# Performance work log

Measured on AMD Instinct MI355X. Metric: run time of the kernel, lower is better.

## Reference

```python
import jax, jax.numpy as jnp
import numpy as np

B, N, D = 2, 2048, 1024
H, DH = 16, 64
INNER = H * DH  # 1024
EPS = 1e-5


def setup_inputs() -> dict:
    key = jax.random.key(0)
    ks = jax.random.split(key, 7)
    x = jax.random.normal(ks[0], (B, N, D), dtype=jnp.float32)
    mask = jax.random.uniform(ks[1], (B, N)) < 0.9
    mask = mask.at[:, 0].set(True)  # guarantee at least one valid key per row
    attn_bias = jax.random.normal(ks[2], (H, N, N), dtype=jnp.float32) * 0.02
    ln_w = jnp.ones((D,), dtype=jnp.float32)
    ln_b = jnp.zeros((D,), dtype=jnp.float32)
    wq = jax.random.normal(ks[3], (D, INNER), dtype=jnp.float32) * 0.02
    wkv = jax.random.normal(ks[4], (D, 2 * DH), dtype=jnp.float32) * 0.02
    wo = jax.random.normal(ks[5], (INNER, D), dtype=jnp.float32) * 0.02
    return {"x": x, "attn_bias": attn_bias, "ln_w": ln_w, "ln_b": ln_b,
            "wq": wq, "wkv": wkv, "wo": wo, "mask": mask}


def reference(x, attn_bias, ln_w, ln_b, wq, wkv, wo, mask):
    scale = DH ** -0.5
    # NOTE: in the torch module, kv_input = x BEFORE self.norm (context=None),
    # so K/V come from raw x while Q comes from LayerNorm(x).
    mu = jnp.mean(x, axis=-1, keepdims=True)
    var = jnp.var(x, axis=-1, keepdims=True)
    xn = (x - mu) / jnp.sqrt(var + EPS) * ln_w + ln_b
    q = (xn @ wq).reshape(B, N, H, DH).transpose(0, 2, 1, 3) * scale  # b h n d
    kv = x @ wkv                     # b n 2*dh (shared single KV head, MQA)
    k, v = kv[..., :DH], kv[..., DH:]
    sim = jnp.einsum('bhid,bjd->bhij', q, k) + attn_bias  # bias broadcasts over b
    mask_value = -jnp.finfo(sim.dtype).max
    sim = jnp.where(mask[:, None, None, :], sim, mask_value)
    attn = jax.nn.softmax(sim, axis=-1)
    out = jnp.einsum('bhij,bjd->bhid', attn, v)
    out = out.transpose(0, 2, 1, 3).reshape(B, N, INNER)
    return out @ wo
```

## Files before the change

### kernel.cpp

```cpp
#include <hip/hip_runtime.h>
#include <hip/hip_bf16.h>

typedef __bf16 bf16_t;
typedef __bf16 bf16x4 __attribute__((ext_vector_type(4)));
typedef __bf16 bf16x8 __attribute__((ext_vector_type(8)));
typedef float f32x4 __attribute__((ext_vector_type(4)));

static constexpr int BB    = 2;
static constexpr int SEQ   = 2048;
static constexpr int DM    = 1024;
static constexpr int NHEAD = 16;
static constexpr int HD    = 64;
static constexpr float L2E = 1.4426950408889634f;

__device__ __forceinline__ bf16x8 ld8(const bf16_t* p) {
  return *reinterpret_cast<const bf16x8*>(p);
}

__device__ __forceinline__ void gl_lds16(const bf16_t* g, bf16_t* l) {
  __builtin_amdgcn_global_load_lds(
      (const __attribute__((address_space(1))) void*)g,
      (__attribute__((address_space(3))) void*)l, 16, 0, 0);
}

template <typename T> __device__ __forceinline__ T cvt_out(float v);
template <> __device__ __forceinline__ float  cvt_out<float >(float v) { return v; }
template <> __device__ __forceinline__ bf16_t cvt_out<bf16_t>(float v) { return (bf16_t)v; }

__global__ __launch_bounds__(256) void transpose_cast(const float* __restrict__ in,
                                                      bf16_t* __restrict__ out,
                                                      int R, int C) {
  __shared__ float tile[32][33];
  const int c0 = blockIdx.x * 32, r0 = blockIdx.y * 32;
  const int tx = threadIdx.x & 31, ty = threadIdx.x >> 5;
#pragma unroll
  for (int y = ty; y < 32; y += 8)
    tile[y][tx] = in[(size_t)(r0 + y) * C + (c0 + tx)];
  __syncthreads();
#pragma unroll
  for (int y = ty; y < 32; y += 8)
    out[(size_t)(c0 + y) * R + (r0 + tx)] = (bf16_t)tile[tx][y];
}

__global__ __launch_bounds__(256) void row_prep(const float* __restrict__ x,
    const float* __restrict__ ln_w, const float* __restrict__ ln_b,
    const int* __restrict__ mask,
    bf16_t* __restrict__ xbf, bf16_t* __restrict__ xn, float* __restrict__ maskA) {
  const int row = blockIdx.x, t = threadIdx.x;
  __shared__ float red[8];
  const float4 xv = *reinterpret_cast<const float4*>(&x[(size_t)row * DM + t * 4]);
  float s  = xv.x + xv.y + xv.z + xv.w;
  float s2 = xv.x * xv.x + xv.y * xv.y + xv.z * xv.z + xv.w * xv.w;
#pragma unroll
  for (int off = 32; off >= 1; off >>= 1) {
    s  += __shfl_xor(s,  off, 64);
    s2 += __shfl_xor(s2, off, 64);
  }
  if ((t & 63) == 0) { red[t >> 6] = s; red[4 + (t >> 6)] = s2; }
  __syncthreads();
  s  = red[0] + red[1] + red[2] + red[3];
  s2 = red[4] + red[5] + red[6] + red[7];
  const float mu   = s * (1.0f / DM);
  const float var  = s2 * (1.0f / DM) - mu * mu;
  const float rstd = rsqrtf(var + 1e-5f);
  const float4 wv = *reinterpret_cast<const float4*>(&ln_w[t * 4]);
  const float4 bv = *reinterpret_cast<const float4*>(&ln_b[t * 4]);
  union { bf16_t h[4]; uint2 u; } p0, p1;
  p0.h[0] = (bf16_t)xv.x; p0.h[1] = (bf16_t)xv.y;
  p0.h[2] = (bf16_t)xv.z; p0.h[3] = (bf16_t)xv.w;
  p1.h[0] = (bf16_t)((xv.x - mu) * rstd * wv.x + bv.x);
  p1.h[1] = (bf16_t)((xv.y - mu) * rstd * wv.y + bv.y);
  p1.h[2] = (bf16_t)((xv.z - mu) * rstd * wv.z + bv.z);
  p1.h[3] = (bf16_t)((xv.w - mu) * rstd * wv.w + bv.w);
  *reinterpret_cast<uint2*>(&xbf[(size_t)row * DM + t * 4]) = p0.u;
  *reinterpret_cast<uint2*>(&xn [(size_t)row * DM + t * 4]) = p1.u;
  if (t == 0) maskA[row] = mask[row] ? 0.0f : -1e30f;
}

template <typename OutT>
__global__ __launch_bounds__(256) void gemm_lds(const bf16_t* __restrict__ A,
    const bf16_t* __restrict__ Bt, OutT* __restrict__ C, OutT* __restrict__ C2,
    int M, int Nn, int K, float scale) {
  __shared__ alignas(16) bf16_t As[128 * 32];
  __shared__ alignas(16) bf16_t Bs[64 * 32];
  const int m0 = blockIdx.x * 128, n0 = blockIdx.y * 64;
  const int t = threadIdx.x, lane = t & 63, w = t >> 6;
  const int wm = (w & 1) * 64, wn = (w >> 1) * 32;
  const int l15 = lane & 15, q4 = lane >> 4;
  f32x4 acc[4][2] = {};
  const int sr = lane >> 2, sc = (lane & 3) * 8;
  const bf16_t* Ap0 = A  + (size_t)(m0 + w * 32 + sr) * K + sc;
  const bf16_t* Ap1 = Ap0 + (size_t)16 * K;
  const bf16_t* Bp  = Bt + (size_t)(n0 + w * 16 + sr) * K + sc;
  bf16_t* AsL0 = &As[(w * 32) * 32];
  bf16_t* AsL1 = &As[(w * 32 + 16) * 32];
  bf16_t* BsL  = &Bs[(w * 16) * 32];
  for (int k0 = 0; k0 < K; k0 += 32) {
    gl_lds16(Ap0 + k0, AsL0);
    gl_lds16(Ap1 + k0, AsL1);
    gl_lds16(Bp  + k0, BsL);
    __syncthreads();
    bf16x8 af[4], bfr[2];
#pragma unroll
    for (int mt = 0; mt < 4; ++mt) af[mt]  = ld8(&As[(wm + mt * 16 + l15) * 32 + q4 * 8]);
#pragma unroll
    for (int nt = 0; nt < 2; ++nt) bfr[nt] = ld8(&Bs[(wn + nt * 16 + l15) * 32 + q4 * 8]);
#pragma unroll
    for (int mt = 0; mt < 4; ++mt)
#pragma unroll
      for (int nt = 0; nt < 2; ++nt)
        acc[mt][nt] = __builtin_amdgcn_mfma_f32_16x16x32_bf16(af[mt], bfr[nt], acc[mt][nt], 0, 0, 0);
    __syncthreads();
  }
#pragma unroll
  for (int mt = 0; mt < 4; ++mt)
#pragma unroll
    for (int nt = 0; nt < 2; ++nt)
#pragma unroll
      for (int r = 0; r < 4; ++r) {
        const int gm = m0 + wm + mt * 16 + q4 * 4 + r;
        const int gn = n0 + wn + nt * 16 + l15;
        const OutT ov = cvt_out<OutT>(acc[mt][nt][r] * scale);
        if (C2 == nullptr) {
          C[(size_t)gm * Nn + gn] = ov;
        } else if (gn < HD) {
          C[(size_t)gm * HD + gn] = ov;
        } else {
          C2[((size_t)(gm >> 11) * HD + (gn - HD)) * SEQ + (gm & 2047)] = ov;
        }
      }
}

__global__ __launch_bounds__(256) void flash_attn(
    const bf16_t* __restrict__ q,
    const bf16_t* __restrict__ kk,
    const bf16_t* __restrict__ vT,
    const float*  __restrict__ bias,
    const float*  __restrict__ maskA,
    bf16_t* __restrict__ aout)
{
  const int b = blockIdx.y & 1, h = blockIdx.y >> 1;
  const int i0 = blockIdx.x * 64;
  const int t = threadIdx.x, lane = t & 63, w = t >> 6;
  const int l15 = lane & 15, q4 = lane >> 4;

  __shared__ alignas(16) bf16_t Qs[64][72];
  __shared__ alignas(16) bf16_t Ks[64][72];
  __shared__ alignas(16) bf16_t Vs[64][72];
  __shared__ alignas(16) bf16_t Pt[4][16][72];

  const int sr = t >> 2, sc = (t & 3) * 16;
  {
    const bf16_t* src = &q[((size_t)b * SEQ + i0 + sr) * DM + h * HD + sc];
    *reinterpret_cast<uint4*>(&Qs[sr][sc])     = *reinterpret_cast<const uint4*>(src);
    *reinterpret_cast<uint4*>(&Qs[sr][sc + 8]) = *reinterpret_cast<const uint4*>(src + 8);
  }
  __syncthreads();
  const bf16x8 bq0 = ld8(&Qs[w * 16 + l15][q4 * 8]);
  const bf16x8 bq1 = ld8(&Qs[w * 16 + l15][32 + q4 * 8]);

  f32x4 o[4] = {};
  float m_run = -1e30f, l_run = 0.0f;

  const float* bias_p = bias + (size_t)h * SEQ * SEQ
                      + (size_t)(i0 + w * 16 + l15) * SEQ + q4 * 4;
  const float* mask_p = maskA + b * SEQ + q4 * 4;
  const bf16_t* kp = &kk[((size_t)b * SEQ + sr) * HD + sc];
  const bf16_t* vp = &vT[((size_t)b * HD + sr) * SEQ + sc];

  for (int j0 = 0; j0 < SEQ; j0 += 64) {
    {
      const bf16_t* ks = kp + (size_t)j0 * HD;
      *reinterpret_cast<uint4*>(&Ks[sr][sc])     = *reinterpret_cast<const uint4*>(ks);
      *reinterpret_cast<uint4*>(&Ks[sr][sc + 8]) = *reinterpret_cast<const uint4*>(ks + 8);
      const bf16_t* vs = vp + j0;
      *reinterpret_cast<uint4*>(&Vs[sr][sc])     = *reinterpret_cast<const uint4*>(vs);
      *reinterpret_cast<uint4*>(&Vs[sr][sc + 8]) = *reinterpret_cast<const uint4*>(vs + 8);
    }
    f32x4 bv[4], mv[4];
#pragma unroll
    for (int mt = 0; mt < 4; ++mt) {
      bv[mt] = *reinterpret_cast<const f32x4*>(bias_p + j0 + mt * 16);
      mv[mt] = *reinterpret_cast<const f32x4*>(mask_p + j0 + mt * 16);
    }
    __syncthreads();

    f32x4 s[4];
#pragma unroll
    for (int mt = 0; mt < 4; ++mt) {
      const bf16x8 a0 = ld8(&Ks[mt * 16 + l15][q4 * 8]);
      const bf16x8 a1 = ld8(&Ks[mt * 16 + l15][32 + q4 * 8]);
      f32x4 z = {0.f, 0.f, 0.f, 0.f};
      z = __builtin_amdgcn_mfma_f32_16x16x32_bf16(a0, bq0, z, 0, 0, 0);
      z = __builtin_amdgcn_mfma_f32_16x16x32_bf16(a1, bq1, z, 0, 0, 0);
      s[mt] = z;
    }

    float mx = -1e30f;
#pragma unroll
    for (int mt = 0; mt < 4; ++mt)
#pragma unroll
      for (int r = 0; r < 4; ++r) {
        s[mt][r] = s[mt][r] + bv[mt][r] + mv[mt][r];
        mx = fmaxf(mx, s[mt][r]);
      }
    mx = fmaxf(mx, __shfl_xor(mx, 16, 64));
    mx = fmaxf(mx, __shfl_xor(mx, 32, 64));
    const float mnew  = fmaxf(m_run, mx);
    const float alpha = __builtin_amdgcn_exp2f((m_run - mnew) * L2E);
    const float cc    = -mnew * L2E;
    m_run = mnew;

    float su = 0.0f;
#pragma unroll
    for (int mt = 0; mt < 4; ++mt)
#pragma unroll
      for (int r = 0; r < 4; ++r) {
        s[mt][r] = __builtin_amdgcn_exp2f(__builtin_fmaf(s[mt][r], L2E, cc));
        su += s[mt][r];
      }
    su += __shfl_xor(su, 16, 64);
    su += __shfl_xor(su, 32, 64);
    l_run = l_run * alpha + su;

#pragma unroll
    for (int mt = 0; mt < 4; ++mt) {
      bf16x4 pk = {(bf16_t)s[mt][0], (bf16_t)s[mt][1], (bf16_t)s[mt][2], (bf16_t)s[mt][3]};
      *reinterpret_cast<bf16x4*>(&Pt[w][l15][mt * 16 + q4 * 4]) = pk;
    }

#pragma unroll
    for (int r = 0; r < 4; ++r) {
      const float a_r = __shfl(alpha, (q4 << 2) + r, 64);
      o[0][r] *= a_r; o[1][r] *= a_r; o[2][r] *= a_r; o[3][r] *= a_r;
    }

#pragma unroll
    for (int ks = 0; ks < 2; ++ks) {
      const bf16x8 pf = ld8(&Pt[w][l15][ks * 32 + q4 * 8]);
#pragma unroll
      for (int nt = 0; nt < 4; ++nt) {
        const bf16x8 vv = ld8(&Vs[nt * 16 + l15][ks * 32 + q4 * 8]);
        o[nt] = __builtin_amdgcn_mfma_f32_16x16x32_bf16(pf, vv, o[nt], 0, 0, 0);
      }
    }
    __syncthreads();
  }

#pragma unroll
  for (int r = 0; r < 4; ++r) {
    const float linv = 1.0f / __shfl(l_run, (q4 << 2) + r, 64);
    const int gi = i0 + w * 16 + q4 * 4 + r;
    bf16_t* dst = &aout[((size_t)b * SEQ + gi) * DM + h * HD];
#pragma unroll
    for (int nt = 0; nt < 4; ++nt)
      dst[nt * 16 + l15] = (bf16_t)(o[nt][r] * linv);
  }
}

extern "C" void kernel_launch(void* const* d_in, const int* in_sizes, int n_in,
                              void* d_out, int out_size, void* d_ws, size_t ws_size,
                              hipStream_t stream) {
  const float* x         = (const float*)d_in[0];
  const float* attn_bias = (const float*)d_in[1];
  const float* ln_w      = (const float*)d_in[2];
  const float* ln_b      = (const float*)d_in[3];
  const float* wq        = (const float*)d_in[4];
  const float* wkv       = (const float*)d_in[5];
  const float* wo        = (const float*)d_in[6];
  const int*   mask      = (const int*)d_in[7];
  float* out = (float*)d_out;

  char* ws = (char*)d_ws;
  size_t off = 0;
  auto alloc = [&](size_t bytes) {
    char* p = ws + off;
    off += (bytes + 255) & ~(size_t)255;
    return p;
  };
  bf16_t* xbf   = (bf16_t*)alloc((size_t)BB * SEQ * DM * 2);
  bf16_t* xn    = (bf16_t*)alloc((size_t)BB * SEQ * DM * 2);
  bf16_t* wqT   = (bf16_t*)alloc((size_t)DM * DM * 2);
  bf16_t* wkvT  = (bf16_t*)alloc((size_t)2 * HD * DM * 2);
  bf16_t* woT   = (bf16_t*)alloc((size_t)DM * DM * 2);
  bf16_t* qb    = (bf16_t*)alloc((size_t)BB * SEQ * DM * 2);
  bf16_t* kkb   = (bf16_t*)alloc((size_t)BB * SEQ * HD * 2);
  bf16_t* vTb   = (bf16_t*)alloc((size_t)BB * HD * SEQ * 2);
  bf16_t* aoutb = (bf16_t*)alloc((size_t)BB * SEQ * DM * 2);
  float*  maskA = (float*)alloc((size_t)BB * SEQ * 4);

  transpose_cast<<<dim3(DM / 32, DM / 32), 256, 0, stream>>>(wq, wqT, DM, DM);
  transpose_cast<<<dim3(128 / 32, DM / 32), 256, 0, stream>>>(wkv, wkvT, DM, 128);
  transpose_cast<<<dim3(DM / 32, DM / 32), 256, 0, stream>>>(wo, woT, DM, DM);
  row_prep<<<BB * SEQ, 256, 0, stream>>>(x, ln_w, ln_b, mask, xbf, xn, maskA);
  gemm_lds<bf16_t><<<dim3(32, 16), 256, 0, stream>>>(xn, wqT, qb, (bf16_t*)nullptr,
                                                     BB * SEQ, DM, DM, 0.125f);
  gemm_lds<bf16_t><<<dim3(32, 2), 256, 0, stream>>>(xbf, wkvT, kkb, vTb,
                                                    BB * SEQ, 128, DM, 1.0f);
  flash_attn<<<dim3(SEQ / 64, BB * NHEAD), 256, 0, stream>>>(qb, kkb, vTb, attn_bias,
                                                             maskA, aoutb);
  gemm_lds<float><<<dim3(32, 16), 256, 0, stream>>>(aoutb, woT, out, (float*)nullptr,
                                                    BB * SEQ, DM, DM, 1.0f);
}
```

Baseline: 525.9 us.

## Double-buffer K/V in flash attention, shuffle P in registers, widen GEMM tiles

New measurement: 512.2 us. -2.6%, faster.

```diff
diff --git a/kernel.cpp b/kernel.cpp
--- a/kernel.cpp
+++ b/kernel.cpp
@@ -21,6 +21,13 @@
   __builtin_amdgcn_global_load_lds(
       (const __attribute__((address_space(1))) void*)g,
       (__attribute__((address_space(3))) void*)l, 16, 0, 0);
+}
+
+__device__ __forceinline__ uint2 shfl2(uint2 v, int src) {
+  uint2 r;
+  r.x = (unsigned)__shfl((int)v.x, src, 64);
+  r.y = (unsigned)__shfl((int)v.y, src, 64);
+  return r;
 }
 
 template <typename T> __device__ __forceinline__ T cvt_out(float v);
@@ -78,9 +85,58 @@
 }
 
 template <typename OutT>
-__global__ __launch_bounds__(256) void gemm_lds(const bf16_t* __restrict__ A,
-    const bf16_t* __restrict__ Bt, OutT* __restrict__ C, OutT* __restrict__ C2,
+__global__ __launch_bounds__(256) void gemm128(const bf16_t* __restrict__ A,
+    const bf16_t* __restrict__ Bt, OutT* __restrict__ C,
     int M, int Nn, int K, float scale) {
+  __shared__ alignas(16) bf16_t As[128 * 32];
+  __shared__ alignas(16) bf16_t Bs[128 * 32];
+  const int m0 = blockIdx.x * 128, n0 = blockIdx.y * 128;
+  const int t = threadIdx.x, lane = t & 63, w = t >> 6;
+  const int wm = (w & 1) * 64, wn = (w >> 1) * 64;
+  const int l15 = lane & 15, q4 = lane >> 4;
+  f32x4 acc[4][4] = {};
+  const int sr = lane >> 2, sc = (lane & 3) * 8;
+  const bf16_t* Ap0 = A  + (size_t)(m0 + w * 32 + sr) * K + sc;
+  const bf16_t* Ap1 = Ap0 + (size_t)16 * K;
+  const bf16_t* Bp0 = Bt + (size_t)(n0 + w * 32 + sr) * K + sc;
+  const bf16_t* Bp1 = Bp0 + (size_t)16 * K;
+  bf16_t* AsL0 = &As[(w * 32) * 32];
+  bf16_t* AsL1 = &As[(w * 32 + 16) * 32];
+  bf16_t* BsL0 = &Bs[(w * 32) * 32];
+  bf16_t* BsL1 = &Bs[(w * 32 + 16) * 32];
+  for (int k0 = 0; k0 < K; k0 += 32) {
+    gl_lds16(Ap0 + k0, AsL0);
+    gl_lds16(Ap1 + k0, AsL1);
+    gl_lds16(Bp0 + k0, BsL0);
+    gl_lds16(Bp1 + k0, BsL1);
+    __syncthreads();
+    bf16x8 af[4], bfr[4];
+#pragma unroll
+    for (int mt = 0; mt < 4; ++mt) af[mt]  = ld8(&As[(wm + mt * 16 + l15) * 32 + q4 * 8]);
+#pragma unroll
+    for (int nt = 0; nt < 4; ++nt) bfr[nt] = ld8(&Bs[(wn + nt * 16 + l15) * 32 + q4 * 8]);
+#pragma unroll
+    for (int mt = 0; mt < 4; ++mt)
+#pragma unroll
+      for (int nt = 0; nt < 4; ++nt)
+        acc[mt][nt] = __builtin_amdgcn_mfma_f32_16x16x32_bf16(af[mt], bfr[nt], acc[mt][nt], 0, 0, 0);
+    __syncthreads();
+  }
+#pragma unroll
+  for (int mt = 0; mt < 4; ++mt)
+#pragma unroll
+    for (int nt = 0; nt < 4; ++nt)
+#pragma unroll
+      for (int r = 0; r < 4; ++r) {
+        const int gm = m0 + wm + mt * 16 + q4 * 4 + r;
+        const int gn = n0 + wn + nt * 16 + l15;
+        C[(size_t)gm * Nn + gn] = cvt_out<OutT>(acc[mt][nt][r] * scale);
+      }
+}
+
+__global__ __launch_bounds__(256) void gemm_kv(const bf16_t* __restrict__ A,
+    const bf16_t* __restrict__ Bt, bf16_t* __restrict__ C, bf16_t* __restrict__ C2,
+    int M, int Nn, int K) {
   __shared__ alignas(16) bf16_t As[128 * 32];
   __shared__ alignas(16) bf16_t Bs[64 * 32];
   const int m0 = blockIdx.x * 128, n0 = blockIdx.y * 64;
@@ -120,18 +176,13 @@
       for (int r = 0; r < 4; ++r) {
         const int gm = m0 + wm + mt * 16 + q4 * 4 + r;
         const int gn = n0 + wn + nt * 16 + l15;
-        const OutT ov = cvt_out<OutT>(acc[mt][nt][r] * scale);
-        if (C2 == nullptr) {
-          C[(size_t)gm * Nn + gn] = ov;
-        } else if (gn < HD) {
-          C[(size_t)gm * HD + gn] = ov;
-        } else {
-          C2[((size_t)(gm >> 11) * HD + (gn - HD)) * SEQ + (gm & 2047)] = ov;
-        }
-      }
-}
-
-__global__ __launch_bounds__(256) void flash_attn(
+        const bf16_t ov = (bf16_t)acc[mt][nt][r];
+        if (gn < HD) C[(size_t)gm * HD + gn] = ov;
+        else C2[((size_t)(gm >> 11) * HD + (gn - HD)) * SEQ + (gm & 2047)] = ov;
+      }
+}
+
+__global__ __launch_bounds__(256, 4) void flash_attn(
     const bf16_t* __restrict__ q,
     const bf16_t* __restrict__ kk,
     const bf16_t* __restrict__ vT,
@@ -144,20 +195,12 @@
   const int t = threadIdx.x, lane = t & 63, w = t >> 6;
   const int l15 = lane & 15, q4 = lane >> 4;
 
-  __shared__ alignas(16) bf16_t Qs[64][72];
-  __shared__ alignas(16) bf16_t Ks[64][72];
-  __shared__ alignas(16) bf16_t Vs[64][72];
-  __shared__ alignas(16) bf16_t Pt[4][16][72];
-
-  const int sr = t >> 2, sc = (t & 3) * 16;
-  {
-    const bf16_t* src = &q[((size_t)b * SEQ + i0 + sr) * DM + h * HD + sc];
-    *reinterpret_cast<uint4*>(&Qs[sr][sc])     = *reinterpret_cast<const uint4*>(src);
-    *reinterpret_cast<uint4*>(&Qs[sr][sc + 8]) = *reinterpret_cast<const uint4*>(src + 8);
-  }
-  __syncthreads();
-  const bf16x8 bq0 = ld8(&Qs[w * 16 + l15][q4 * 8]);
-  const bf16x8 bq1 = ld8(&Qs[w * 16 + l15][32 + q4 * 8]);
+  __shared__ alignas(16) bf16_t Ks[2][64][72];
+  __shared__ alignas(16) bf16_t Vs[2][64][72];
+
+  const bf16_t* qrow = &q[((size_t)b * SEQ + i0 + w * 16 + l15) * DM + h * HD];
+  const bf16x8 bq0 = ld8(qrow + q4 * 8);
+  const bf16x8 bq1 = ld8(qrow + 32 + q4 * 8);
 
   f32x4 o[4] = {};
   float m_run = -1e30f, l_run = 0.0f;
@@ -165,31 +208,43 @@
   const float* bias_p = bias + (size_t)h * SEQ * SEQ
                       + (size_t)(i0 + w * 16 + l15) * SEQ + q4 * 4;
   const float* mask_p = maskA + b * SEQ + q4 * 4;
+
+  const int sr = t >> 2, sc = (t & 3) * 16;
   const bf16_t* kp = &kk[((size_t)b * SEQ + sr) * HD + sc];
   const bf16_t* vp = &vT[((size_t)b * HD + sr) * SEQ + sc];
 
-  for (int j0 = 0; j0 < SEQ; j0 += 64) {
-    {
-      const bf16_t* ks = kp + (size_t)j0 * HD;
-      *reinterpret_cast<uint4*>(&Ks[sr][sc])     = *reinterpret_cast<const uint4*>(ks);
-      *reinterpret_cast<uint4*>(&Ks[sr][sc + 8]) = *reinterpret_cast<const uint4*>(ks + 8);
-      const bf16_t* vs = vp + j0;
-      *reinterpret_cast<uint4*>(&Vs[sr][sc])     = *reinterpret_cast<const uint4*>(vs);
-      *reinterpret_cast<uint4*>(&Vs[sr][sc + 8]) = *reinterpret_cast<const uint4*>(vs + 8);
-    }
-    f32x4 bv[4], mv[4];
+  uint4 kr0 = *reinterpret_cast<const uint4*>(kp);
+  uint4 kr1 = *reinterpret_cast<const uint4*>(kp + 8);
+  uint4 vr0 = *reinterpret_cast<const uint4*>(vp);
+  uint4 vr1 = *reinterpret_cast<const uint4*>(vp + 8);
+  f32x4 bv[4], mv[4];
+#pragma unroll
+  for (int mt = 0; mt < 4; ++mt) {
+    bv[mt] = *reinterpret_cast<const f32x4*>(bias_p + mt * 16);
+    mv[mt] = *reinterpret_cast<const f32x4*>(mask_p + mt * 16);
+  }
+  *reinterpret_cast<uint4*>(&Ks[0][sr][sc])     = kr0;
+  *reinterpret_cast<uint4*>(&Ks[0][sr][sc + 8]) = kr1;
+  *reinterpret_cast<uint4*>(&Vs[0][sr][sc])     = vr0;
+  *reinterpret_cast<uint4*>(&Vs[0][sr][sc + 8]) = vr1;
+  __syncthreads();
+
+  for (int it = 0; it < SEQ / 64; ++it) {
+    const int buf = it & 1;
+    const int j1 = (it + 1) * 64;
+    const bool more = (j1 < SEQ);
+    if (more) {
+      kr0 = *reinterpret_cast<const uint4*>(kp + (size_t)j1 * HD);
+      kr1 = *reinterpret_cast<const uint4*>(kp + (size_t)j1 * HD + 8);
+      vr0 = *reinterpret_cast<const uint4*>(vp + j1);
+      vr1 = *reinterpret_cast<const uint4*>(vp + j1 + 8);
+    }
+
+    f32x4 s[4];
 #pragma unroll
     for (int mt = 0; mt < 4; ++mt) {
-      bv[mt] = *reinterpret_cast<const f32x4*>(bias_p + j0 + mt * 16);
-      mv[mt] = *reinterpret_cast<const f32x4*>(mask_p + j0 + mt * 16);
-    }
-    __syncthreads();
-
-    f32x4 s[4];
-#pragma unroll
-    for (int mt = 0; mt < 4; ++mt) {
-      const bf16x8 a0 = ld8(&Ks[mt * 16 + l15][q4 * 8]);
-      const bf16x8 a1 = ld8(&Ks[mt * 16 + l15][32 + q4 * 8]);
+      const bf16x8 a0 = ld8(&Ks[buf][mt * 16 + l15][q4 * 8]);
+      const bf16x8 a1 = ld8(&Ks[buf][mt * 16 + l15][32 + q4 * 8]);
       f32x4 z = {0.f, 0.f, 0.f, 0.f};
       z = __builtin_amdgcn_mfma_f32_16x16x32_bf16(a0, bq0, z, 0, 0, 0);
       z = __builtin_amdgcn_mfma_f32_16x16x32_bf16(a1, bq1, z, 0, 0, 0);
@@ -204,6 +259,13 @@
         s[mt][r] = s[mt][r] + bv[mt][r] + mv[mt][r];
         mx = fmaxf(mx, s[mt][r]);
       }
+    if (more) {
+#pragma unroll
+      for (int mt = 0; mt < 4; ++mt) {
+        bv[mt] = *reinterpret_cast<const f32x4*>(bias_p + j1 + mt * 16);
+        mv[mt] = *reinterpret_cast<const f32x4*>(mask_p + j1 + mt * 16);
+      }
+    }
     mx = fmaxf(mx, __shfl_xor(mx, 16, 64));
     mx = fmaxf(mx, __shfl_xor(mx, 32, 64));
     const float mnew  = fmaxf(m_run, mx);
@@ -224,32 +286,50 @@
     l_run = l_run * alpha + su;
 
 #pragma unroll
+    for (int r = 0; r < 4; ++r) {
+      const float a_r = __shfl(alpha, q4 * 4 + r, 64);
+      o[0][r] *= a_r; o[1][r] *= a_r; o[2][r] *= a_r; o[3][r] *= a_r;
+    }
+
+    uint2 pk[4];
+#pragma unroll
     for (int mt = 0; mt < 4; ++mt) {
-      bf16x4 pk = {(bf16_t)s[mt][0], (bf16_t)s[mt][1], (bf16_t)s[mt][2], (bf16_t)s[mt][3]};
-      *reinterpret_cast<bf16x4*>(&Pt[w][l15][mt * 16 + q4 * 4]) = pk;
-    }
-
-#pragma unroll
-    for (int r = 0; r < 4; ++r) {
-      const float a_r = __shfl(alpha, (q4 << 2) + r, 64);
-      o[0][r] *= a_r; o[1][r] *= a_r; o[2][r] *= a_r; o[3][r] *= a_r;
-    }
-
+      union { bf16_t hh[4]; uint2 u; } pu;
+      pu.hh[0] = (bf16_t)s[mt][0]; pu.hh[1] = (bf16_t)s[mt][1];
+      pu.hh[2] = (bf16_t)s[mt][2]; pu.hh[3] = (bf16_t)s[mt][3];
+      pk[mt] = pu.u;
+    }
+    const int src0 = ((q4 & 1) << 5) + l15;
+    const int src1 = src0 + 16;
+    const bool hiSel = (q4 >> 1) != 0;
 #pragma unroll
     for (int ks = 0; ks < 2; ++ks) {
-      const bf16x8 pf = ld8(&Pt[w][l15][ks * 32 + q4 * 8]);
+      const uint2 a0 = shfl2(pk[2 * ks],     src0);
+      const uint2 a1 = shfl2(pk[2 * ks + 1], src0);
+      const uint2 b0 = shfl2(pk[2 * ks],     src1);
+      const uint2 b1 = shfl2(pk[2 * ks + 1], src1);
+      union { unsigned u[4]; bf16x8 v; } pf;
+      pf.u[0] = hiSel ? a1.x : a0.x; pf.u[1] = hiSel ? a1.y : a0.y;
+      pf.u[2] = hiSel ? b1.x : b0.x; pf.u[3] = hiSel ? b1.y : b0.y;
 #pragma unroll
       for (int nt = 0; nt < 4; ++nt) {
-        const bf16x8 vv = ld8(&Vs[nt * 16 + l15][ks * 32 + q4 * 8]);
-        o[nt] = __builtin_amdgcn_mfma_f32_16x16x32_bf16(pf, vv, o[nt], 0, 0, 0);
-      }
+        const bf16x8 vv = ld8(&Vs[buf][nt * 16 + l15][ks * 32 + q4 * 8]);
+        o[nt] = __builtin_amdgcn_mfma_f32_16x16x32_bf16(pf.v, vv, o[nt], 0, 0, 0);
+      }
+    }
+
+    if (more) {
+      *reinterpret_cast<uint4*>(&Ks[buf ^ 1][sr][sc])     = kr0;
+      *reinterpret_cast<uint4*>(&Ks[buf ^ 1][sr][sc + 8]) = kr1;
+      *reinterpret_cast<uint4*>(&Vs[buf ^ 1][sr][sc])     = vr0;
+      *reinterpret_cast<uint4*>(&Vs[buf ^ 1][sr][sc + 8]) = vr1;
     }
     __syncthreads();
   }
 
 #pragma unroll
   for (int r = 0; r < 4; ++r) {
-    const float linv = 1.0f / __shfl(l_run, (q4 << 2) + r, 64);
+    const float linv = 1.0f / __shfl(l_run, q4 * 4 + r, 64);
     const int gi = i0 + w * 16 + q4 * 4 + r;
     bf16_t* dst = &aout[((size_t)b * SEQ + gi) * DM + h * HD];
 #pragma unroll
@@ -293,12 +373,9 @@
   transpose_cast<<<dim3(128 / 32, DM / 32), 256, 0, stream>>>(wkv, wkvT, DM, 128);
   transpose_cast<<<dim3(DM / 32, DM / 32), 256, 0, stream>>>(wo, woT, DM, DM);
   row_prep<<<BB * SEQ, 256, 0, stream>>>(x, ln_w, ln_b, mask, xbf, xn, maskA);
-  gemm_lds<bf16_t><<<dim3(32, 16), 256, 0, stream>>>(xn, wqT, qb, (bf16_t*)nullptr,
-                                                     BB * SEQ, DM, DM, 0.125f);
-  gemm_lds<bf16_t><<<dim3(32, 2), 256, 0, stream>>>(xbf, wkvT, kkb, vTb,
-                                                    BB * SEQ, 128, DM, 1.0f);
+  gemm128<bf16_t><<<dim3(32, 8), 256, 0, stream>>>(xn, wqT, qb, BB * SEQ, DM, DM, 0.125f);
+  gemm_kv<<<dim3(32, 2), 256, 0, stream>>>(xbf, wkvT, kkb, vTb, BB * SEQ, 128, DM);
   flash_attn<<<dim3(SEQ / 64, BB * NHEAD), 256, 0, stream>>>(qb, kkb, vTb, attn_bias,
                                                              maskA, aoutb);
-  gemm_lds<float><<<dim3(32, 16), 256, 0, stream>>>(aoutb, woT, out, (float*)nullptr,
-                                                    BB * SEQ, DM, DM, 1.0f);
-}
+  gemm128<float><<<dim3(32, 8), 256, 0, stream>>>(aoutb, woT, out, BB * SEQ, DM, DM, 1.0f);
+}
```
